# Kernel tuning notes

Measured on AMD Instinct MI355X. Metric: run time of the kernel, lower is better.

The kernel has to match this reference:

```python
import jax, jax.numpy as jnp
import numpy as np

N_SAMPLES = 16_777_216  # total surviving samples across all rays
N_RAY = 65_536          # number of rays


def setup_inputs() -> dict:
    key = jax.random.key(0)
    k1, k2 = jax.random.split(key)
    alpha = jax.random.uniform(k1, (N_SAMPLES,), dtype=jnp.float32)
    # sorted ray ids -> contiguous segments, as produced by create_full_step_id + masking
    ray_id = jnp.sort(jax.random.randint(k2, (N_SAMPLES,), 0, N_RAY, dtype=jnp.int32))
    return {"alpha": alpha, "ray_id": ray_id, "N_ray": N_RAY}


def _seg_prod_op(a, b):
    # segmented-product combine: reset the running product at segment starts
    va, fa = a
    vb, fb = b
    return jnp.where(fb, vb, va * vb), fa | fb


def reference(alpha, ray_id, N_ray):
    n = alpha.shape[0]
    one_minus_alpha = 1.0 - alpha + 1e-11                      # [n]
    is_start = jnp.concatenate(
        [jnp.ones((1,), jnp.bool_), ray_id[1:] != ray_id[:-1]]
    )                                                          # [n] segment starts
    # parallel segmented cumulative product (replaces the per-sample Python loop)
    cumprod, _ = jax.lax.associative_scan(_seg_prod_op, (one_minus_alpha, is_start))
    # NOTE: faithful to the source: transmittance is a global shift of cumprod
    # (cat([1, cumprod[:-1]])), NOT reset to 1 at each ray start.
    transmittance = jnp.concatenate([jnp.ones((1,), alpha.dtype), cumprod[:-1]])
    weights = alpha * transmittance                            # [n]
    # last sample index of each ray (ids are sorted, so max index == last write)
    last_idx = jnp.zeros((N_ray,), jnp.int32).at[ray_id].max(
        jnp.arange(n, dtype=jnp.int32)
    )                                                          # [N_ray]
    alphainv_last = cumprod[last_idx]                          # [N_ray]
    return weights, alphainv_last
```

## Files before the change

### kernel.cpp

```cpp
#include <hip/hip_runtime.h>
#include <stdint.h>


#define BLOCK 256
#define NWAVE (BLOCK / 64)
#define NJ 4
#define WELEM (64 * 4 * NJ)
#define CHUNK (NWAVE * WELEM)

struct Pair { float v; int f; };

__device__ __forceinline__ Pair seg_combine(Pair a, Pair b) {
    Pair r;
    r.v = b.f ? b.v : (a.v * b.v);
    r.f = a.f | b.f;
    return r;
}

__device__ __forceinline__ Pair wave_scan_incl(Pair x, int lane) {
    #pragma unroll
    for (int off = 1; off < 64; off <<= 1) {
        Pair o;
        o.v = __shfl_up(x.v, off);
        o.f = __shfl_up(x.f, off);
        if (lane >= off) x = seg_combine(o, x);
    }
    return x;
}

__global__ __launch_bounds__(BLOCK)
void nerf_reduce(const float* __restrict__ alpha, const int* __restrict__ ray_id,
                 float2* __restrict__ agg, float* __restrict__ alphainv,
                 int N_ray, int n) {
    const int c = blockIdx.x, t = threadIdx.x;
    const int lane = t & 63, w = t >> 6;
    const long wbase = (long)c * CHUNK + (long)w * WELEM;

    {
        int gid = c * BLOCK + t;
        if (gid < N_ray) alphainv[gid] = (1.0f - alpha[0]) + 1e-11f;
    }

    int last_r = -1;
    if (wbase > 0 && wbase - 1 < (long)n) last_r = ray_id[wbase - 1];

    Pair wrun; wrun.v = 1.0f; wrun.f = 0;
    #pragma unroll
    for (int j = 0; j < NJ; ++j) {
        const long e0 = wbase + j * 256 + lane * 4;
        float4 av; int4 rv;
        if (e0 + 4 <= (long)n) {
            av = *(const float4*)(alpha  + e0);
            rv = *(const int4*)  (ray_id + e0);
        } else {
            float aa[4]; int rr[4];
            for (int k = 0; k < 4; ++k) {
                long g = e0 + k;
                aa[k] = (g < n) ? alpha[g]  : 0.0f;
                rr[k] = (g < n) ? ray_id[g] : -2;
            }
            av = make_float4(aa[0], aa[1], aa[2], aa[3]);
            rv = make_int4(rr[0], rr[1], rr[2], rr[3]);
        }
        const bool b0 = e0 < n, b1 = e0 + 1 < n, b2 = e0 + 2 < n, b3 = e0 + 3 < n;
        const float om0 = b0 ? (1.0f - av.x) + 1e-11f : 1.0f;
        const float om1 = b1 ? (1.0f - av.y) + 1e-11f : 1.0f;
        const float om2 = b2 ? (1.0f - av.z) + 1e-11f : 1.0f;
        const float om3 = b3 ? (1.0f - av.w) + 1e-11f : 1.0f;
        const int up = __shfl_up(rv.w, 1);
        const int prev0 = (lane == 0) ? last_r : up;
        const int f0 = b0 && (rv.x != prev0);
        const int f1 = b1 && (rv.y != rv.x);
        const int f2 = b2 && (rv.z != rv.y);
        const int f3 = b3 && (rv.w != rv.z);

        Pair l; l.v = om0; l.f = f0;
        { Pair e; e.v = om1; e.f = f1; l = seg_combine(l, e); }
        { Pair e; e.v = om2; e.f = f2; l = seg_combine(l, e); }
        { Pair e; e.v = om3; e.f = f3; l = seg_combine(l, e); }

        Pair ws = wave_scan_incl(l, lane);
        Pair jag; jag.v = __shfl(ws.v, 63); jag.f = __shfl(ws.f, 63);
        wrun = seg_combine(wrun, jag);
        last_r = __shfl(rv.w, 63);
    }

    __shared__ float s_wv[NWAVE];
    __shared__ int   s_wf[NWAVE];
    if (lane == 0) { s_wv[w] = wrun.v; s_wf[w] = wrun.f; }
    __syncthreads();
    if (t == 0) {
        Pair acc; acc.v = s_wv[0]; acc.f = s_wf[0];
        #pragma unroll
        for (int ww = 1; ww < NWAVE; ++ww) {
            Pair e; e.v = s_wv[ww]; e.f = s_wf[ww];
            acc = seg_combine(acc, e);
        }
        agg[c] = make_float2(acc.v, __int_as_float(acc.f));
    }
}

__global__ __launch_bounds__(BLOCK)
void nerf_apply(const float* __restrict__ alpha, const int* __restrict__ ray_id,
                const float2* __restrict__ agg,
                float* __restrict__ weights, float* __restrict__ alphainv, int n) {
    __shared__ float s_wv[NWAVE];
    __shared__ int   s_wf[NWAVE];
    __shared__ float s_pv;
    __shared__ int   s_pf;

    const int c = blockIdx.x, t = threadIdx.x;
    const int lane = t & 63, w = t >> 6;
    const long wbase = (long)c * CHUNK + (long)w * WELEM;

    if (t == 0) {
        Pair pre; pre.v = 1.0f; pre.f = 0;
        for (int j = c - 1; j >= 0; --j) {
            float2 g = agg[j];
            Pair e; e.v = g.x; e.f = __float_as_int(g.y);
            pre = (j == c - 1) ? e : seg_combine(e, pre);
            if (pre.f) break;
        }
        s_pv = pre.v; s_pf = pre.f;
    }

    int last_r = -1;
    if (wbase > 0 && wbase - 1 < (long)n) last_r = ray_id[wbase - 1];

    float4 A[NJ]; int4 R[NJ]; Pair E[NJ]; int PR0[NJ];
    Pair wrun; wrun.v = 1.0f; wrun.f = 0;

    #pragma unroll
    for (int j = 0; j < NJ; ++j) {
        const long e0 = wbase + j * 256 + lane * 4;
        if (e0 + 4 <= (long)n) {
            A[j] = *(const float4*)(alpha  + e0);
            R[j] = *(const int4*)  (ray_id + e0);
        } else {
            float aa[4]; int rr[4];
            for (int k = 0; k < 4; ++k) {
                long g = e0 + k;
                aa[k] = (g < n) ? alpha[g]  : 0.0f;
                rr[k] = (g < n) ? ray_id[g] : -2;
            }
            A[j] = make_float4(aa[0], aa[1], aa[2], aa[3]);
            R[j] = make_int4(rr[0], rr[1], rr[2], rr[3]);
        }
        const float4 av = A[j]; const int4 rv = R[j];
        const bool b0 = e0 < n, b1 = e0 + 1 < n, b2 = e0 + 2 < n, b3 = e0 + 3 < n;
        const float om0 = b0 ? (1.0f - av.x) + 1e-11f : 1.0f;
        const float om1 = b1 ? (1.0f - av.y) + 1e-11f : 1.0f;
        const float om2 = b2 ? (1.0f - av.z) + 1e-11f : 1.0f;
        const float om3 = b3 ? (1.0f - av.w) + 1e-11f : 1.0f;
        const int up = __shfl_up(rv.w, 1);
        const int prev0 = (lane == 0) ? last_r : up;
        PR0[j] = prev0;
        const int f0 = b0 && (rv.x != prev0);
        const int f1 = b1 && (rv.y != rv.x);
        const int f2 = b2 && (rv.z != rv.y);
        const int f3 = b3 && (rv.w != rv.z);

        Pair l; l.v = om0; l.f = f0;
        { Pair e; e.v = om1; e.f = f1; l = seg_combine(l, e); }
        { Pair e; e.v = om2; e.f = f2; l = seg_combine(l, e); }
        { Pair e; e.v = om3; e.f = f3; l = seg_combine(l, e); }

        Pair ws = wave_scan_incl(l, lane);
        Pair wse;
        {
            float uv = __shfl_up(ws.v, 1);
            int   uf = __shfl_up(ws.f, 1);
            if (lane == 0) { wse.v = 1.0f; wse.f = 0; }
            else           { wse.v = uv;   wse.f = uf; }
        }
        E[j] = seg_combine(wrun, wse);
        Pair jag; jag.v = __shfl(ws.v, 63); jag.f = __shfl(ws.f, 63);
        wrun = seg_combine(wrun, jag);
        last_r = __shfl(rv.w, 63);
    }

    if (lane == 0) { s_wv[w] = wrun.v; s_wf[w] = wrun.f; }
    __syncthreads();

    Pair base; base.v = s_pv; base.f = s_pf;
    for (int ww = 0; ww < w; ++ww) {
        Pair e; e.v = s_wv[ww]; e.f = s_wf[ww];
        base = seg_combine(base, e);
    }

    #pragma unroll
    for (int j = 0; j < NJ; ++j) {
        Pair P = seg_combine(base, E[j]);
        const float4 av = A[j]; const int4 rv = R[j];
        const long e0 = wbase + j * 256 + lane * 4;
        const bool b0 = e0 < n, b1 = e0 + 1 < n, b2 = e0 + 2 < n, b3 = e0 + 3 < n;
        const float om0 = b0 ? (1.0f - av.x) + 1e-11f : 1.0f;
        const float om1 = b1 ? (1.0f - av.y) + 1e-11f : 1.0f;
        const float om2 = b2 ? (1.0f - av.z) + 1e-11f : 1.0f;
        const float om3 = b3 ? (1.0f - av.w) + 1e-11f : 1.0f;
        const int prev0 = PR0[j];
        const int f0 = b0 && (rv.x != prev0);
        const int f1 = b1 && (rv.y != rv.x);
        const int f2 = b2 && (rv.z != rv.y);
        const int f3 = b3 && (rv.w != rv.z);

        float w0, w1, w2, w3;
        w0 = av.x * P.v;
        if (f0 && e0 > 0) alphainv[prev0] = P.v;
        { Pair e; e.v = om0; e.f = f0; P = seg_combine(P, e); }
        if (b0 && e0 == (long)n - 1) alphainv[rv.x] = P.v;
        w1 = av.y * P.v;
        if (f1) alphainv[rv.x] = P.v;
        { Pair e; e.v = om1; e.f = f1; P = seg_combine(P, e); }
        if (b1 && e0 + 1 == (long)n - 1) alphainv[rv.y] = P.v;
        w2 = av.z * P.v;
        if (f2) alphainv[rv.y] = P.v;
        { Pair e; e.v = om2; e.f = f2; P = seg_combine(P, e); }
        if (b2 && e0 + 2 == (long)n - 1) alphainv[rv.z] = P.v;
        w3 = av.w * P.v;
        if (f3) alphainv[rv.z] = P.v;
        { Pair e; e.v = om3; e.f = f3; P = seg_combine(P, e); }
        if (b3 && e0 + 3 == (long)n - 1) alphainv[rv.w] = P.v;

        if (e0 + 4 <= (long)n) {
            *(float4*)(weights + e0) = make_float4(w0, w1, w2, w3);
        } else {
            float ww4[4] = {w0, w1, w2, w3};
            for (int k = 0; k < 4; ++k) {
                long g = e0 + k;
                if (g < n) weights[g] = ww4[k];
            }
        }
    }
}

extern "C" void kernel_launch(void* const* d_in, const int* in_sizes, int n_in,
                              void* d_out, int out_size, void* d_ws, size_t ws_size,
                              hipStream_t stream) {
    const float* alpha  = (const float*)d_in[0];
    const int*   ray_id = (const int*)d_in[1];
    const int n     = in_sizes[0];
    const int N_ray = out_size - n;

    float* weights  = (float*)d_out;
    float* alphainv = weights + n;
    float2* agg     = (float2*)d_ws;

    const int nchunks = (n + CHUNK - 1) / CHUNK;

    nerf_reduce<<<nchunks, BLOCK, 0, stream>>>(alpha, ray_id, agg, alphainv, N_ray, n);
    if (N_ray > nchunks * BLOCK) {
        int extra = N_ray - nchunks * BLOCK;
        nerf_reduce<<<0, 0, 0, stream>>>(alpha, ray_id, agg, alphainv, 0, 0);
        (void)extra;
    }
    nerf_apply<<<nchunks, BLOCK, 0, stream>>>(alpha, ray_id, agg, weights, alphainv, n);
}
```

Before: 201.4 us.

## Replace reduce+apply scan with single-pass kernel using local segment lookback

```diff
diff --git a/kernel.cpp b/kernel.cpp
--- a/kernel.cpp
+++ b/kernel.cpp
@@ -7,6 +7,7 @@
 #define NJ 4
 #define WELEM (64 * 4 * NJ)
 #define CHUNK (NWAVE * WELEM)
+#define LOOKW 1024
 
 struct Pair { float v; int f; };
 
@@ -28,100 +29,67 @@
     return x;
 }
 
-__global__ __launch_bounds__(BLOCK)
-void nerf_reduce(const float* __restrict__ alpha, const int* __restrict__ ray_id,
-                 float2* __restrict__ agg, float* __restrict__ alphainv,
-                 int N_ray, int n) {
-    const int c = blockIdx.x, t = threadIdx.x;
-    const int lane = t & 63, w = t >> 6;
-    const long wbase = (long)c * CHUNK + (long)w * WELEM;
-
-    {
-        int gid = c * BLOCK + t;
-        if (gid < N_ray) alphainv[gid] = (1.0f - alpha[0]) + 1e-11f;
-    }
-
-    int last_r = -1;
-    if (wbase > 0 && wbase - 1 < (long)n) last_r = ray_id[wbase - 1];
-
-    Pair wrun; wrun.v = 1.0f; wrun.f = 0;
-    #pragma unroll
-    for (int j = 0; j < NJ; ++j) {
-        const long e0 = wbase + j * 256 + lane * 4;
-        float4 av; int4 rv;
-        if (e0 + 4 <= (long)n) {
-            av = *(const float4*)(alpha  + e0);
-            rv = *(const int4*)  (ray_id + e0);
-        } else {
-            float aa[4]; int rr[4];
-            for (int k = 0; k < 4; ++k) {
-                long g = e0 + k;
-                aa[k] = (g < n) ? alpha[g]  : 0.0f;
-                rr[k] = (g < n) ? ray_id[g] : -2;
-            }
-            av = make_float4(aa[0], aa[1], aa[2], aa[3]);
-            rv = make_int4(rr[0], rr[1], rr[2], rr[3]);
-        }
-        const bool b0 = e0 < n, b1 = e0 + 1 < n, b2 = e0 + 2 < n, b3 = e0 + 3 < n;
-        const float om0 = b0 ? (1.0f - av.x) + 1e-11f : 1.0f;
-        const float om1 = b1 ? (1.0f - av.y) + 1e-11f : 1.0f;
-        const float om2 = b2 ? (1.0f - av.z) + 1e-11f : 1.0f;
-        const float om3 = b3 ? (1.0f - av.w) + 1e-11f : 1.0f;
-        const int up = __shfl_up(rv.w, 1);
-        const int prev0 = (lane == 0) ? last_r : up;
-        const int f0 = b0 && (rv.x != prev0);
-        const int f1 = b1 && (rv.y != rv.x);
-        const int f2 = b2 && (rv.z != rv.y);
-        const int f3 = b3 && (rv.w != rv.z);
-
-        Pair l; l.v = om0; l.f = f0;
-        { Pair e; e.v = om1; e.f = f1; l = seg_combine(l, e); }
-        { Pair e; e.v = om2; e.f = f2; l = seg_combine(l, e); }
-        { Pair e; e.v = om3; e.f = f3; l = seg_combine(l, e); }
-
-        Pair ws = wave_scan_incl(l, lane);
-        Pair jag; jag.v = __shfl(ws.v, 63); jag.f = __shfl(ws.f, 63);
-        wrun = seg_combine(wrun, jag);
-        last_r = __shfl(rv.w, 63);
-    }
-
-    __shared__ float s_wv[NWAVE];
-    __shared__ int   s_wf[NWAVE];
-    if (lane == 0) { s_wv[w] = wrun.v; s_wf[w] = wrun.f; }
-    __syncthreads();
-    if (t == 0) {
-        Pair acc; acc.v = s_wv[0]; acc.f = s_wf[0];
-        #pragma unroll
-        for (int ww = 1; ww < NWAVE; ++ww) {
-            Pair e; e.v = s_wv[ww]; e.f = s_wf[ww];
-            acc = seg_combine(acc, e);
-        }
-        agg[c] = make_float2(acc.v, __int_as_float(acc.f));
-    }
-}
-
-__global__ __launch_bounds__(BLOCK)
-void nerf_apply(const float* __restrict__ alpha, const int* __restrict__ ray_id,
-                const float2* __restrict__ agg,
+__global__ void nerf_init(const float* __restrict__ alpha,
+                          float* __restrict__ alphainv, int N_ray) {
+    int i = blockIdx.x * blockDim.x + threadIdx.x;
+    if (i < N_ray) alphainv[i] = (1.0f - alpha[0]) + 1e-11f;
+}
+
+__global__ __launch_bounds__(BLOCK, 4)
+void nerf_fused(const float* __restrict__ alpha, const int* __restrict__ ray_id,
                 float* __restrict__ weights, float* __restrict__ alphainv, int n) {
     __shared__ float s_wv[NWAVE];
     __shared__ int   s_wf[NWAVE];
-    __shared__ float s_pv;
-    __shared__ int   s_pf;
+    __shared__ int   s_rid[BLOCK];
+    __shared__ float s_bv;
+    __shared__ int   s_bf;
 
     const int c = blockIdx.x, t = threadIdx.x;
     const int lane = t & 63, w = t >> 6;
-    const long wbase = (long)c * CHUNK + (long)w * WELEM;
-
-    if (t == 0) {
-        Pair pre; pre.v = 1.0f; pre.f = 0;
-        for (int j = c - 1; j >= 0; --j) {
-            float2 g = agg[j];
-            Pair e; e.v = g.x; e.f = __float_as_int(g.y);
-            pre = (j == c - 1) ? e : seg_combine(e, pre);
-            if (pre.f) break;
-        }
-        s_pv = pre.v; s_pf = pre.f;
+    const long bstart = (long)c * CHUNK;
+    const long wbase  = bstart + (long)w * WELEM;
+
+    float P0 = 1.0f;
+    if (c > 0) {
+        long wlo = bstart - LOOKW;
+        Pair chain; chain.v = 1.0f; chain.f = 0;
+        for (;;) {
+            const long e0 = wlo + 4 * t;
+            float4 av = *(const float4*)(alpha  + e0);
+            int4   rv = *(const int4*)  (ray_id + e0);
+            s_rid[t] = rv.w;
+            __syncthreads();
+            const int prev = (t == 0) ? ((wlo > 0) ? ray_id[wlo - 1] : -1) : s_rid[t - 1];
+            Pair l;
+            l.v = (1.0f - av.x) + 1e-11f; l.f = (rv.x != prev);
+            { Pair e; e.v = (1.0f - av.y) + 1e-11f; e.f = (rv.y != rv.x); l = seg_combine(l, e); }
+            { Pair e; e.v = (1.0f - av.z) + 1e-11f; e.f = (rv.z != rv.y); l = seg_combine(l, e); }
+            { Pair e; e.v = (1.0f - av.w) + 1e-11f; e.f = (rv.w != rv.z); l = seg_combine(l, e); }
+            #pragma unroll
+            for (int off = 1; off < 64; off <<= 1) {
+                Pair o;
+                o.v = __shfl_down(l.v, off);
+                o.f = __shfl_down(l.f, off);
+                l = seg_combine(l, o);
+            }
+            if (lane == 0) { s_wv[w] = l.v; s_wf[w] = l.f; }
+            __syncthreads();
+            if (t == 0) {
+                Pair acc; acc.v = s_wv[0]; acc.f = s_wf[0];
+                #pragma unroll
+                for (int ww = 1; ww < NWAVE; ++ww) {
+                    Pair e; e.v = s_wv[ww]; e.f = s_wf[ww];
+                    acc = seg_combine(acc, e);
+                }
+                s_bv = acc.v; s_bf = acc.f;
+            }
+            __syncthreads();
+            Pair wagg; wagg.v = s_bv; wagg.f = s_bf;
+            chain = seg_combine(wagg, chain);
+            if (chain.f || wlo == 0) break;
+            wlo -= LOOKW;
+        }
+        P0 = chain.v;
     }
 
     int last_r = -1;
@@ -182,7 +150,7 @@
     if (lane == 0) { s_wv[w] = wrun.v; s_wf[w] = wrun.f; }
     __syncthreads();
 
-    Pair base; base.v = s_pv; base.f = s_pf;
+    Pair base; base.v = P0; base.f = (c > 0);
     for (int ww = 0; ww < w; ++ww) {
         Pair e; e.v = s_wv[ww]; e.f = s_wf[ww];
         base = seg_combine(base, e);
@@ -244,15 +212,9 @@
 
     float* weights  = (float*)d_out;
     float* alphainv = weights + n;
-    float2* agg     = (float2*)d_ws;
 
     const int nchunks = (n + CHUNK - 1) / CHUNK;
 
-    nerf_reduce<<<nchunks, BLOCK, 0, stream>>>(alpha, ray_id, agg, alphainv, N_ray, n);
-    if (N_ray > nchunks * BLOCK) {
-        int extra = N_ray - nchunks * BLOCK;
-        nerf_reduce<<<0, 0, 0, stream>>>(alpha, ray_id, agg, alphainv, 0, 0);
-        (void)extra;
-    }
-    nerf_apply<<<nchunks, BLOCK, 0, stream>>>(alpha, ray_id, agg, weights, alphainv, n);
-}
+    nerf_init<<<(N_ray + BLOCK - 1) / BLOCK, BLOCK, 0, stream>>>(alpha, alphainv, N_ray);
+    nerf_fused<<<nchunks, BLOCK, 0, stream>>>(alpha, ray_id, weights, alphainv, n);
+}
```

New measurement: 179.3 us. 11.0% less time.
